# Performance work log

Measured on AMD Instinct MI355X. Metric: run time of the kernel, lower is better.

The kernel has to match this reference:

```python
import jax, jax.numpy as jnp
import numpy as np

N_INST, BATCH, IN_DIM, L_DIM = 256, 128, 1024, 512

def setup_inputs() -> dict:
    key = jax.random.key(0)
    k1, k2, k3, k4 = jax.random.split(key, 4)
    # glorot-uniform-ish scales
    sv = np.sqrt(6.0 / (IN_DIM + L_DIM)).astype(np.float32)
    sw = np.sqrt(6.0 / (L_DIM + 1)).astype(np.float32)
    x = jax.random.normal(k1, (N_INST, BATCH, IN_DIM), dtype=jnp.float32)
    v = jax.random.uniform(k2, (IN_DIM, L_DIM), minval=-sv, maxval=sv, dtype=jnp.float32)
    u = jax.random.uniform(k3, (IN_DIM, L_DIM), minval=-sv, maxval=sv, dtype=jnp.float32)
    w = jax.random.uniform(k4, (L_DIM, 1), minval=-sw, maxval=sw, dtype=jnp.float32)
    return {"x": x, "v": v, "u": u, "w": w}

def reference(x, v, u, w):
    # x: [n_instances, batch, in_dim]
    # Fused batched version of the per-instance loop:
    # score_i = (tanh(x_i @ v) * sigmoid(x_i @ u)) @ w, softmax over instances.
    h = jnp.tanh(jnp.einsum('nbd,dl->nbl', x, v))          # [n, b, l]
    g = jax.nn.sigmoid(jnp.einsum('nbd,dl->nbl', x, u))    # [n, b, l]
    scores = jnp.einsum('nbl,lo->nbo', h * g, w)            # [n, b, 1]
    alpha = jax.nn.softmax(scores, axis=0)                  # softmax over instance axis
    return alpha
```

## Files before the change

kernel.cpp:

```cpp
#include <hip/hip_runtime.h>
#include <stdint.h>

typedef unsigned int  u32;
typedef unsigned short u16;
typedef __bf16 v8bf __attribute__((ext_vector_type(8)));
typedef float  v4f  __attribute__((ext_vector_type(4)));

#define N_INST 256
#define BATCH  128
#define IN_DIM 1024
#define L_DIM  512
#define M_TOT  (N_INST*BATCH)
#define NSLICE 16

#define XB_BYTES   ((size_t)M_TOT * IN_DIM * 2)
#define WPK_BYTES  ((size_t)1024 * IN_DIM * 2)

__device__ inline u32 f2bf_pk(float a, float b){
  u32 ua = __builtin_bit_cast(u32, a);
  u32 ub = __builtin_bit_cast(u32, b);
  ua = (ua + 0x7FFFu + ((ua >> 16) & 1u)) >> 16;
  ub = (ub + 0x7FFFu + ((ub >> 16) & 1u)) & 0xFFFF0000u;
  return ua | ub;
}

__device__ inline void gl2lds16(const u16* g, u16* l){
  __builtin_amdgcn_global_load_lds(
      (const __attribute__((address_space(1))) u32*)(g),
      (__attribute__((address_space(3))) u32*)(l), 16, 0, 0);
}

#define PREP_XBLKS 16384
__global__ void prep(const float* __restrict__ x, const float* __restrict__ v,
                     const float* __restrict__ u, u16* __restrict__ xb,
                     u16* __restrict__ wpk){
  const int b = blockIdx.x;
  if (b < PREP_XBLKS){
    int t = b * 256 + threadIdx.x;
    int r = t >> 6, l = t & 63;
    int kk = r & 1, i = (r >> 1) & 3, h = (r >> 3) & 1, kt = (r >> 4) & 15, mb = r >> 8;
    int q = l >> 4, c = l & 15;
    int row = mb*128 + h*64 + i*16 + c;
    int k0  = kt*64 + kk*32 + q*8;
    const float* src = x + (size_t)row * IN_DIM + k0;
    float4 a0 = *reinterpret_cast<const float4*>(src);
    float4 a1 = *reinterpret_cast<const float4*>(src + 4);
    uint4 out;
    out.x = f2bf_pk(a0.x, a0.y); out.y = f2bf_pk(a0.z, a0.w);
    out.z = f2bf_pk(a1.x, a1.y); out.w = f2bf_pk(a1.z, a1.w);
    *reinterpret_cast<uint4*>(xb + (size_t)r*512 + l*8) = out;
  } else {
    int t = (b - PREP_XBLKS) * 256 + threadIdx.x;
    int r = t >> 6, l = t & 63;
    int kk = r & 1, j = (r >> 1) & 3, kt = (r >> 3) & 15, cs = r >> 7;
    int q = l >> 4, c = l & 15;
    int bcol = cs*4 + j;
    const float* src = (bcol & 1) ? u : v;
    int lcol = (bcol >> 1)*16 + c;
    int k0 = kt*64 + kk*32 + q*8;
    u32 o[4];
#pragma unroll
    for (int ii = 0; ii < 4; ++ii){
      float a  = src[(size_t)(k0 + 2*ii    ) * L_DIM + lcol];
      float bb = src[(size_t)(k0 + 2*ii + 1) * L_DIM + lcol];
      o[ii] = f2bf_pk(a, bb);
    }
    *reinterpret_cast<uint4*>(wpk + (size_t)r*512 + l*8) = make_uint4(o[0], o[1], o[2], o[3]);
  }
}


#define STAGE_P(KKC, RB) { _Pragma("unroll") for (int it_ = 0; it_ < 3; ++it_)        \
    gl2lds16(sp[it_] + (KKC)*512, &Ls[(RB) + (wave3 + it_)*512]); }

#define STAGE_N(KKC, RB) { _Pragma("unroll") for (int it_ = 0; it_ < 3; ++it_)        \
    gl2lds16(sp[it_] + sstr[it_] + (KKC)*512, &Ls[(RB) + (wave3 + it_)*512]); }

#define FRAGS(RB) {                                                                   \
  _Pragma("unroll") for (int gi_ = 0; gi_ < 4; ++gi_)                                 \
    afb[gi_] = *reinterpret_cast<const v8bf*>(&Ls[(RB) + ao0 + gi_*512]);             \
  _Pragma("unroll") for (int j_ = 0; j_ < 4; ++j_)                                    \
    bfb[j_] = *reinterpret_cast<const v8bf*>(&Ls[(RB) + bo0 + j_*512]); }

#define MFMA16 {                                                                      \
  __builtin_amdgcn_s_setprio(1);                                                      \
  _Pragma("unroll") for (int j_ = 0; j_ < 4; ++j_)                                    \
    _Pragma("unroll") for (int gi_ = 0; gi_ < 4; ++gi_)                               \
      acc[gi_][j_] = __builtin_amdgcn_mfma_f32_16x16x32_bf16(                         \
          afb[gi_], bfb[j_], acc[gi_][j_], 0, 0, 0);                                  \
  __builtin_amdgcn_s_setprio(0); }

#define BARC(N) {                                                                     \
  __builtin_amdgcn_sched_barrier(0);                                                  \
  asm volatile("s_waitcnt vmcnt(" #N ")" ::: "memory");                               \
  __builtin_amdgcn_s_barrier();                                                       \
  __builtin_amdgcn_sched_barrier(0); }

__launch_bounds__(512, 4)
__global__ void gemm_score(const u16* __restrict__ xb, const u16* __restrict__ wpk,
                           const float* __restrict__ w, float* __restrict__ partial){
  __shared__ __align__(16) u16 Ls[3*24*512];

  const int tid  = threadIdx.x;
  const u32 bid  = blockIdx.x;
  const int lo  = bid & 7;
  const int csp = (bid >> 3) & 7;
  const int hi  = bid >> 6;
  const int m   = lo*16 + hi;
  const int mblk0 = m*2;

  const int lane = tid & 63;
  const int wave = tid >> 6;
  const int wave3= wave*3;
  const int q    = lane >> 4;
  const int c    = lane & 15;
  const int wm   = wave >> 1;
  const int wn   = wave & 1;

  const u16* sp[3]; u32 sstr[3];
#pragma unroll
  for (int it = 0; it < 3; ++it){
    int r = wave3 + it;
    if (r < 16){
      sp[it]   = xb + ((size_t)(mblk0 + (r>>3))*256 + (r&7)*2)*512 + lane*8;
      sstr[it] = 16*512;
    } else {
      int rb_ = r - 16;
      sp[it]   = wpk + ((size_t)((csp*2 + (rb_>>2))*128 + (rb_&3)*2))*512 + lane*8;
      sstr[it] = 8*512;
    }
  }

  const u32 ao0 = (u32)(((wm>>1)*8 + (wm&1)*4)*512) + lane*8;
  const u32 bo0 = (u32)((16 + wn*4)*512) + lane*8;

  v8bf afb[4];
  v8bf bfb[4];
  v4f  acc[4][4];
#pragma unroll
  for (int gi = 0; gi < 4; ++gi)
#pragma unroll
    for (int j = 0; j < 4; ++j)
      acc[gi][j] = (v4f){0.f, 0.f, 0.f, 0.f};

  u32 rb0 = 0, rb1 = 12288, rb2 = 24576;

  STAGE_P(0, rb0);
  STAGE_P(1, rb1);
  BARC(3);

#pragma unroll 1
  for (int kt = 0; kt < 15; ++kt){
    STAGE_N(0, rb2);
    FRAGS(rb0);
    MFMA16;
    BARC(3);
    STAGE_N(1, rb0);
    FRAGS(rb1);
    MFMA16;
    BARC(3);
    { u32 t = rb0; rb0 = rb2; rb2 = rb1; rb1 = t; }
#pragma unroll
    for (int it = 0; it < 3; ++it) sp[it] += sstr[it];
  }
  FRAGS(rb0);
  MFMA16;
  BARC(0);
  FRAGS(rb1);
  MFMA16;

  const int cs = csp*2 + wn;
  const float wl0 = w[cs*32 + c];
  const float wl1 = w[cs*32 + 16 + c];
  float* pout = partial + (size_t)cs * M_TOT + (size_t)m*256 + wm*64;

#pragma unroll
  for (int gi = 0; gi < 4; ++gi){
#pragma unroll
    for (int r = 0; r < 4; ++r){
      float t0 = 2.f / (1.f + __expf(-2.f * acc[gi][0][r])) - 1.f;
      float s0 = 1.f / (1.f + __expf(-acc[gi][1][r]));
      float t1 = 2.f / (1.f + __expf(-2.f * acc[gi][2][r])) - 1.f;
      float s1 = 1.f / (1.f + __expf(-acc[gi][3][r]));
      float v2 = t0*s0*wl0 + t1*s1*wl1;
      v2 += __shfl_xor(v2, 1, 64);
      v2 += __shfl_xor(v2, 2, 64);
      v2 += __shfl_xor(v2, 4, 64);
      v2 += __shfl_xor(v2, 8, 64);
      if (c == 0) pout[gi*16 + q*4 + r] = v2;
    }
  }
}

__global__ void softmax_inst(const float* __restrict__ partial, float* __restrict__ out){
  __shared__ float red[N_INST];
  const int b = blockIdx.x;
  const int n = threadIdx.x;
  float s = 0.f;
#pragma unroll
  for (int i = 0; i < NSLICE; ++i) s += partial[(size_t)i * M_TOT + n*BATCH + b];
  red[n] = s; __syncthreads();
  for (int st = N_INST/2; st > 0; st >>= 1){
    if (n < st) red[n] = fmaxf(red[n], red[n + st]);
    __syncthreads();
  }
  float mx = red[0]; __syncthreads();
  float e = __expf(s - mx);
  red[n] = e; __syncthreads();
  for (int st = N_INST/2; st > 0; st >>= 1){
    if (n < st) red[n] += red[n + st];
    __syncthreads();
  }
  out[n*BATCH + b] = e / red[0];
}

extern "C" void kernel_launch(void* const* d_in, const int* in_sizes, int n_in,
                              void* d_out, int out_size, void* d_ws, size_t ws_size,
                              hipStream_t stream) {
  const float* x = (const float*)d_in[0];
  const float* v = (const float*)d_in[1];
  const float* u = (const float*)d_in[2];
  const float* w = (const float*)d_in[3];
  u16*   xb      = (u16*)d_ws;
  u16*   wpk     = (u16*)((char*)d_ws + XB_BYTES);
  float* partial = (float*)((char*)d_ws + XB_BYTES + WPK_BYTES);
  float* out     = (float*)d_out;

  prep<<<dim3(PREP_XBLKS + 512), dim3(256), 0, stream>>>(x, v, u, xb, wpk);
  gemm_score<<<dim3(1024), dim3(512), 0, stream>>>(xb, wpk, w, partial);
  softmax_inst<<<dim3(BATCH), dim3(N_INST), 0, stream>>>(partial, out);
}
```

Measured before the change: 288.1 us.

## Shrink GEMM block tile to 128x128 with 4 waves and 2048 blocks

Changes the gemm_score block tile from 256 rows by 128 columns (8 waves, 512 threads) to 128 rows by 128 columns (4 waves, 256 threads). The LDS staging is reorganized so each wave loads 4 chunks per stage, and the grid doubles to 2048 blocks. The aim is more blocks and better SM balance with a smaller LDS footprint. In exchange the x tile is reused across fewer columns, so more global and L2 traffic per FLOP.

Result: no change. 289.9 us (+0.6%).

```diff
diff --git a/kernel.cpp b/kernel.cpp
--- a/kernel.cpp
+++ b/kernel.cpp
@@ -70,11 +70,8 @@
 }
 
 
-#define STAGE_P(KKC, RB) { _Pragma("unroll") for (int it_ = 0; it_ < 3; ++it_)        \
-    gl2lds16(sp[it_] + (KKC)*512, &Ls[(RB) + (wave3 + it_)*512]); }
-
-#define STAGE_N(KKC, RB) { _Pragma("unroll") for (int it_ = 0; it_ < 3; ++it_)        \
-    gl2lds16(sp[it_] + sstr[it_] + (KKC)*512, &Ls[(RB) + (wave3 + it_)*512]); }
+#define STAGE(SP, RB) { _Pragma("unroll") for (int it_ = 0; it_ < 4; ++it_)           \
+    gl2lds16((SP) + it_*1024, &Ls[(RB) + dst0 + it_*512]); }
 
 #define FRAGS(RB) {                                                                   \
   _Pragma("unroll") for (int gi_ = 0; gi_ < 4; ++gi_)                                 \
@@ -96,43 +93,40 @@
   __builtin_amdgcn_s_barrier();                                                       \
   __builtin_amdgcn_sched_barrier(0); }
 
-__launch_bounds__(512, 4)
+__launch_bounds__(256, 3)
 __global__ void gemm_score(const u16* __restrict__ xb, const u16* __restrict__ wpk,
                            const float* __restrict__ w, float* __restrict__ partial){
-  __shared__ __align__(16) u16 Ls[3*24*512];
+  __shared__ __align__(16) u16 Ls[3*16*512];
 
   const int tid  = threadIdx.x;
   const u32 bid  = blockIdx.x;
   const int lo  = bid & 7;
   const int csp = (bid >> 3) & 7;
   const int hi  = bid >> 6;
-  const int m   = lo*16 + hi;
-  const int mblk0 = m*2;
+  const int mblk = lo*32 + hi;
 
   const int lane = tid & 63;
   const int wave = tid >> 6;
-  const int wave3= wave*3;
   const int q    = lane >> 4;
   const int c    = lane & 15;
   const int wm   = wave >> 1;
   const int wn   = wave & 1;
 
-  const u16* sp[3]; u32 sstr[3];
-#pragma unroll
-  for (int it = 0; it < 3; ++it){
-    int r = wave3 + it;
-    if (r < 16){
-      sp[it]   = xb + ((size_t)(mblk0 + (r>>3))*256 + (r&7)*2)*512 + lane*8;
-      sstr[it] = 16*512;
-    } else {
-      int rb_ = r - 16;
-      sp[it]   = wpk + ((size_t)((csp*2 + (rb_>>2))*128 + (rb_&3)*2))*512 + lane*8;
-      sstr[it] = 8*512;
-    }
-  }
-
-  const u32 ao0 = (u32)(((wm>>1)*8 + (wm&1)*4)*512) + lane*8;
-  const u32 bo0 = (u32)((16 + wn*4)*512) + lane*8;
+  const u16* sbase;
+  u32 astep;
+  if (wave < 2){
+    sbase = xb + ((size_t)mblk*256 + (size_t)wave*8)*512 + lane*8;
+    astep = 16*512;
+  } else {
+    sbase = wpk + ((size_t)(csp*2 + (wave-2))*128)*512 + lane*8;
+    astep = 8*512;
+  }
+  const u16* spA = sbase;
+  const u16* spB = sbase + 512;
+
+  const u32 dst0 = (u32)(wave*4)*512;
+  const u32 ao0  = (u32)(wm*4)*512 + lane*8;
+  const u32 bo0  = (u32)(8 + wn*4)*512 + lane*8;
 
   v8bf afb[4];
   v8bf bfb[4];
@@ -143,25 +137,23 @@
     for (int j = 0; j < 4; ++j)
       acc[gi][j] = (v4f){0.f, 0.f, 0.f, 0.f};
 
-  u32 rb0 = 0, rb1 = 12288, rb2 = 24576;
-
-  STAGE_P(0, rb0);
-  STAGE_P(1, rb1);
-  BARC(3);
+  u32 rb0 = 0, rb1 = 8192, rb2 = 16384;
+
+  STAGE(spA, rb0); spA += astep;
+  STAGE(spB, rb1); spB += astep;
+  BARC(4);
 
 #pragma unroll 1
   for (int kt = 0; kt < 15; ++kt){
-    STAGE_N(0, rb2);
+    STAGE(spA, rb2); spA += astep;
     FRAGS(rb0);
     MFMA16;
-    BARC(3);
-    STAGE_N(1, rb0);
+    BARC(4);
+    STAGE(spB, rb0); spB += astep;
     FRAGS(rb1);
     MFMA16;
-    BARC(3);
+    BARC(4);
     { u32 t = rb0; rb0 = rb2; rb2 = rb1; rb1 = t; }
-#pragma unroll
-    for (int it = 0; it < 3; ++it) sp[it] += sstr[it];
   }
   FRAGS(rb0);
   MFMA16;
@@ -172,7 +164,7 @@
   const int cs = csp*2 + wn;
   const float wl0 = w[cs*32 + c];
   const float wl1 = w[cs*32 + 16 + c];
-  float* pout = partial + (size_t)cs * M_TOT + (size_t)m*256 + wm*64;
+  float* pout = partial + (size_t)cs * M_TOT + (size_t)mblk*128 + wm*64;
 
 #pragma unroll
   for (int gi = 0; gi < 4; ++gi){
@@ -227,6 +219,6 @@
   float* out     = (float*)d_out;
 
   prep<<<dim3(PREP_XBLKS + 512), dim3(256), 0, stream>>>(x, v, u, xb, wpk);
-  gemm_score<<<dim3(1024), dim3(512), 0, stream>>>(xb, wpk, w, partial);
+  gemm_score<<<dim3(2048), dim3(256), 0, stream>>>(xb, wpk, w, partial);
   softmax_inst<<<dim3(BATCH), dim3(N_INST), 0, stream>>>(partial, out);
 }
```
